# Performance work log

Measured on AMD Instinct MI355X. Metric: run time of the kernel, lower is better.

Reference implementation:

```python
import jax, jax.numpy as jnp
import numpy as np

N_ROLES = 6
EPS = 1e-5

def _ln(x, scale, bias):
    m = jnp.mean(x, axis=-1, keepdims=True)
    v = jnp.var(x, axis=-1, keepdims=True)
    return (x - m) * jax.lax.rsqrt(v + EPS) * scale + bias

def setup_inputs() -> dict:
    key = jax.random.key(0)
    ks = jax.random.split(key, 20)
    T, B, D_OBS, H, A = 32, 1024, 256, 512, 32
    inp = {
        'rnn_states': jax.random.normal(ks[0], (B, H), jnp.float32),
        'obs': jax.random.normal(ks[1], (T, B, D_OBS), jnp.float32),
        'resets': jnp.zeros((T, B), jnp.float32),
        'available_actions': jnp.ones((T, B, A), jnp.float32),
        'role_ids': jax.random.randint(ks[2], (T, B), 0, N_ROLES, jnp.int32),
        # feature norm over obs_dim
        'fn_scale': jnp.ones((D_OBS,), jnp.float32),
        'fn_bias': jnp.zeros((D_OBS,), jnp.float32),
        # base MLP: obs_dim->512->512, each followed by LayerNorm
        'W0': jax.random.normal(ks[3], (D_OBS, H), jnp.float32) * 0.02,
        'b0': jnp.zeros((H,), jnp.float32),
        'ln0_scale': jnp.ones((H,), jnp.float32),
        'ln0_bias': jnp.zeros((H,), jnp.float32),
        'W1': jax.random.normal(ks[4], (H, H), jnp.float32) * 0.02,
        'b1': jnp.zeros((H,), jnp.float32),
        'ln1_scale': jnp.ones((H,), jnp.float32),
        'ln1_bias': jnp.zeros((H,), jnp.float32),
        # per-role routes: obs_dim->128->H (stacked over roles)
        'Wr0': jax.random.normal(ks[5], (N_ROLES, D_OBS, 128), jnp.float32) * 0.02,
        'br0': jnp.zeros((N_ROLES, 128), jnp.float32),
        'Wr1': jax.random.normal(ks[6], (N_ROLES, 128, H), jnp.float32) * 0.02,
        'br1': jnp.zeros((N_ROLES, H), jnp.float32),
        # per-role heads: H->64->32->action_dim (stacked over roles)
        'Wh0': jax.random.normal(ks[7], (N_ROLES, H, 64), jnp.float32) * 0.02,
        'bh0': jnp.zeros((N_ROLES, 64), jnp.float32),
        'Wh1': jax.random.normal(ks[8], (N_ROLES, 64, 32), jnp.float32) * 0.02,
        'bh1': jnp.zeros((N_ROLES, 32), jnp.float32),
        'Wh2': jax.random.normal(ks[9], (N_ROLES, 32, A), jnp.float32) * 0.02,
        'bh2': jnp.zeros((N_ROLES, A), jnp.float32),
    }
    return inp

def _gather_by_role(all_values, role_ids):
    # all_values: (K, T, B, F); role_ids: (T, B) -> (T, B, F)
    idx = role_ids[None, :, :, None].astype(jnp.int32)
    return jnp.take_along_axis(all_values, idx, axis=0)[0]

def reference(rnn_states, obs, resets, available_actions, role_ids,
              fn_scale, fn_bias, W0, b0, ln0_scale, ln0_bias,
              W1, b1, ln1_scale, ln1_bias,
              Wr0, br0, Wr1, br1,
              Wh0, bh0, Wh1, bh1, Wh2, bh2):
    # feature normalization on raw obs
    obs_n = _ln(obs, fn_scale, fn_bias)
    # shared base MLP (relu + LayerNorm after each Dense)
    e = _ln(jax.nn.relu(obs_n @ W0 + b0), ln0_scale, ln0_bias)
    e = _ln(jax.nn.relu(e @ W1 + b1), ln1_scale, ln1_bias)
    # per-role pre-GRU residual routes on (normalized) obs
    r = jax.nn.relu(jnp.einsum('tbi,kih->ktbh', obs_n, Wr0) + br0[:, None, None, :])
    r = jax.nn.relu(jnp.einsum('ktbh,kho->ktbo', r, Wr1) + br1[:, None, None, :])
    e = e + _gather_by_role(r, role_ids)
    # no recurrent policy configured: rnn_states pass through
    # per-role heads -> all logits (K, T, B, A)
    h = jax.nn.relu(jnp.einsum('tbh,khf->ktbf', e, Wh0) + bh0[:, None, None, :])
    h = jax.nn.relu(jnp.einsum('ktbf,kfg->ktbg', h, Wh1) + bh1[:, None, None, :])
    all_logits = jnp.einsum('ktbg,kga->ktba', h, Wh2) + bh2[:, None, None, :]
    logits = _gather_by_role(all_logits, role_ids)
    logits = jnp.where(available_actions > 0.5, logits, jnp.full_like(logits, -1e10))
    return rnn_states, logits
```

## Files before the change

kernel.cpp:

```cpp
#include <hip/hip_runtime.h>
#include <stdint.h>

typedef unsigned short u16;
typedef unsigned int u32;

using bf16x8 = __attribute__((ext_vector_type(8))) short;
using f32x4  = __attribute__((ext_vector_type(4))) float;

#define DEVINL __device__ __forceinline__

DEVINL float b2f(u16 u) { return __builtin_bit_cast(float, (u32)u << 16); }
DEVINL u16 f2b(float f) {
  u32 u = __builtin_bit_cast(u32, f);
  u += 0x7FFFu + ((u >> 16) & 1u);
  return (u16)(u >> 16);
}

DEVINL void gll16(const u16* src, u16* dst) {
  __builtin_amdgcn_global_load_lds(
      (const __attribute__((address_space(1))) void*)(uintptr_t)src,
      (__attribute__((address_space(3))) void*)(uintptr_t)dst, 16, 0, 0);
}

DEVINL void tp_tile(const float* __restrict__ s, u16* __restrict__ d,
                    int R, int C, int bx, int by, int z)
{
  __shared__ u16 tile[32][33];
  const size_t mstride = (size_t)R * C;
  s += (size_t)z * mstride;
  d += (size_t)z * mstride;
  int r0 = bx * 32, c0 = by * 32;
  int tx = threadIdx.x & 31, ty = threadIdx.x >> 5;
#pragma unroll
  for (int i = 0; i < 32; i += 8)
    tile[ty + i][tx] = f2b(s[(size_t)(r0 + ty + i) * C + (c0 + tx)]);
  __syncthreads();
#pragma unroll
  for (int i = 0; i < 32; i += 8)
    d[(size_t)(c0 + ty + i) * R + (r0 + tx)] = tile[tx][ty + i];
}

__global__ __launch_bounds__(256) void transpose_all(
    const float* W0, const float* W1, const float* Wr0, const float* Wr1, const float* Wh0,
    u16* W0t, u16* W1t, u16* Wr0t, u16* Wr1t, u16* Wh0t)
{
  int b = blockIdx.x;
  if (b < 128)      {            tp_tile(W0, W0t, 256, 512, b % 8,  b / 8, 0); }
  else if (b < 384) { b -= 128;  tp_tile(W1, W1t, 512, 512, b % 16, b / 16, 0); }
  else if (b < 576) { b -= 384;  int t = b / 8;  tp_tile(Wr0, Wr0t, 256, 128, b % 8,  t % 4,  t / 4); }
  else if (b < 960) { b -= 576;  int t = b / 4;  tp_tile(Wr1, Wr1t, 128, 512, b % 4,  t % 16, t / 16); }
  else              { b -= 960;  int t = b / 16; tp_tile(Wh0, Wh0t, 512, 64,  b % 16, t % 2,  t / 2); }
}

__global__ __launch_bounds__(256) void ln_f32_256(
    const float* __restrict__ X, const float* __restrict__ sc,
    const float* __restrict__ bi, u16* __restrict__ Y, int nrows)
{
  constexpr int D = 256, PER = 4;
  int lane = threadIdx.x & 63;
  int row = blockIdx.x * 4 + (threadIdx.x >> 6);
  if (row >= nrows) return;
  const float* xr = X + (size_t)row * D + lane * PER;
  float x[PER] __attribute__((aligned(16)));
  *(float4*)x = *(const float4*)xr;
  float s = 0.f, s2 = 0.f;
#pragma unroll
  for (int p = 0; p < PER; ++p) { s += x[p]; s2 += x[p] * x[p]; }
#pragma unroll
  for (int o = 32; o > 0; o >>= 1) { s += __shfl_xor(s, o, 64); s2 += __shfl_xor(s2, o, 64); }
  float m = s * (1.f / D);
  float v = s2 * (1.f / D) - m * m;
  float inv = rsqrtf(v + 1e-5f);
  u16 yu[PER] __attribute__((aligned(8)));
#pragma unroll
  for (int p = 0; p < PER; ++p)
    yu[p] = f2b((x[p] - m) * inv * sc[lane * PER + p] + bi[lane * PER + p]);
  *(uint2*)(Y + (size_t)row * D + lane * PER) = *(uint2*)yu;
}

#define NROLE 6
__global__ __launch_bounds__(256) void role_count(
    const int* __restrict__ rid, int* __restrict__ blkCnt)
{
  __shared__ int h[NROLE];
  if (threadIdx.x < NROLE) h[threadIdx.x] = 0;
  __syncthreads();
  int i = blockIdx.x * 256 + threadIdx.x;
  atomicAdd(&h[rid[i]], 1);
  __syncthreads();
  if (threadIdx.x < NROLE) blkCnt[blockIdx.x * NROLE + threadIdx.x] = h[threadIdx.x];
}

__global__ __launch_bounds__(256) void role_scan(
    const int* __restrict__ blkCnt, int* __restrict__ blkBase,
    int* __restrict__ baseArr, int* __restrict__ cntArr)
{
  __shared__ int c[128 * NROLE];
  __shared__ int bb[128 * NROLE];
  __shared__ int sbase[NROLE], scnt[NROLE];
  for (int i = threadIdx.x; i < 128 * NROLE; i += 256) c[i] = blkCnt[i];
  __syncthreads();
  if (threadIdx.x < NROLE) {
    int k = threadIdx.x, run = 0;
    for (int b = 0; b < 128; ++b) { bb[b * NROLE + k] = run; run += c[b * NROLE + k]; }
    scnt[k] = run;
  }
  __syncthreads();
  if (threadIdx.x == 0) {
    int r = 0;
    for (int k = 0; k < NROLE; ++k) { sbase[k] = r; r += scnt[k]; }
  }
  __syncthreads();
  if (threadIdx.x < NROLE) { baseArr[threadIdx.x] = sbase[threadIdx.x]; cntArr[threadIdx.x] = scnt[threadIdx.x]; }
  for (int i = threadIdx.x; i < 128 * NROLE; i += 256)
    blkBase[i] = bb[i] + sbase[i % NROLE];
}

__global__ __launch_bounds__(256) void role_fill(
    const int* __restrict__ rid, const int* __restrict__ blkBase, int* __restrict__ bucket)
{
  __shared__ int h[NROLE];
  if (threadIdx.x < NROLE) h[threadIdx.x] = 0;
  __syncthreads();
  int i = blockIdx.x * 256 + threadIdx.x;
  int k = rid[i];
  int pos = atomicAdd(&h[k], 1);
  bucket[blkBase[blockIdx.x * NROLE + k] + pos] = i;
}

template <int K>
__global__ __launch_bounds__(256, 4) void gemm_ln(
    const u16* __restrict__ A, const u16* __restrict__ Bt,
    const float* __restrict__ bias, const float* __restrict__ lnsc,
    const float* __restrict__ lnbi, u16* __restrict__ C)
{
  constexpr int BK = 64;
  __shared__ __align__(16) u16 As[32 * BK];
  __shared__ float redS[32][4];
  __shared__ float redSS[32][4];
  __shared__ float prm[1536];
  const int tid = threadIdx.x;
  const int rowBase = blockIdx.x * 32;
  const int lane = tid & 63, wave = tid >> 6;
#pragma unroll
  for (int i = tid; i < 512; i += 256) {
    prm[i] = bias[i]; prm[512 + i] = lnsc[i]; prm[1024 + i] = lnbi[i];
  }
  const int srow = tid >> 3;
  const u32 aOff = (u32)(rowBase + srow) * (u32)K + (u32)(((tid & 7) ^ (srow & 7)) * 8);
  const int quad = lane >> 4, lm = lane & 15, l7 = lm & 7;
  const int wn = wave * 128;
  u32 bOff[8];
#pragma unroll
  for (int j = 0; j < 8; ++j)
    bOff[j] = (u32)(wn + j * 16 + lm) * (u32)K + (u32)(quad * 8);

  f32x4 acc[2][8] = {};

  for (int k0 = 0; k0 < K; k0 += BK) {
    gll16(A + aOff + k0, &As[wave * 512]);
    __syncthreads();
#pragma unroll
    for (int kk = 0; kk < BK; kk += 32) {
      const int kc = kk >> 3;
      bf16x8 af[2], bfr[8];
#pragma unroll
      for (int i2 = 0; i2 < 2; ++i2)
        af[i2] = *(const bf16x8*)&As[(i2 * 16 + lm) * 64 + (((quad + kc) ^ l7) * 8)];
#pragma unroll
      for (int j = 0; j < 8; ++j)
        bfr[j] = *(const bf16x8*)(Bt + bOff[j] + k0 + kk);
#pragma unroll
      for (int i2 = 0; i2 < 2; ++i2)
#pragma unroll
        for (int j = 0; j < 8; ++j)
          acc[i2][j] = __builtin_amdgcn_mfma_f32_16x16x32_bf16(af[i2], bfr[j], acc[i2][j], 0, 0, 0);
    }
    __syncthreads();
  }

#pragma unroll
  for (int i2 = 0; i2 < 2; ++i2) {
#pragma unroll
    for (int r2 = 0; r2 < 4; ++r2) {
      float s = 0.f, ss = 0.f;
#pragma unroll
      for (int j = 0; j < 8; ++j) {
        float v = fmaxf(acc[i2][j][r2] + prm[wn + j * 16 + lm], 0.f);
        acc[i2][j][r2] = v;
        s += v; ss += v * v;
      }
#pragma unroll
      for (int o = 1; o < 16; o <<= 1) { s += __shfl_xor(s, o, 64); ss += __shfl_xor(ss, o, 64); }
      if (lm == 0) {
        int rowL = i2 * 16 + quad * 4 + r2;
        redS[rowL][wave] = s;
        redSS[rowL][wave] = ss;
      }
    }
  }
  __syncthreads();
#pragma unroll
  for (int i2 = 0; i2 < 2; ++i2) {
#pragma unroll
    for (int r2 = 0; r2 < 4; ++r2) {
      int rowL = i2 * 16 + quad * 4 + r2;
      float ts  = redS[rowL][0] + redS[rowL][1] + redS[rowL][2] + redS[rowL][3];
      float tss = redSS[rowL][0] + redSS[rowL][1] + redSS[rowL][2] + redSS[rowL][3];
      float m = ts * (1.f / 512.f);
      float var = tss * (1.f / 512.f) - m * m;
      float inv = rsqrtf(var + 1e-5f);
      size_t base = (size_t)(rowBase + rowL) * 512;
#pragma unroll
      for (int j = 0; j < 8; ++j) {
        int col = wn + j * 16 + lm;
        float y = (acc[i2][j][r2] - m) * inv * prm[512 + col] + prm[1024 + col];
        C[base + col] = f2b(y);
      }
    }
  }
}

__global__ __launch_bounds__(256, 3) void route_head(
    const u16* __restrict__ obs_n, const u16* __restrict__ e,
    const u16* __restrict__ Wr0t, const float* __restrict__ br0,
    const u16* __restrict__ Wr1t, const float* __restrict__ br1,
    const u16* __restrict__ Wh0t, const float* __restrict__ bh0,
    const int* __restrict__ bucket, const int* __restrict__ baseArr,
    const int* __restrict__ cntArr, u16* __restrict__ h0buf)
{
  __shared__ __align__(16) u16 sm[20480];
  __shared__ float prm[704];
  const int tid = threadIdx.x;

  int role = 0, rem = blockIdx.x, cnt;
  for (;;) {
    cnt = cntArr[role];
    int tiles = (cnt + 31) >> 5;
    if (rem < tiles) break;
    rem -= tiles;
    if (++role >= NROLE) return;
  }
  const int limit = cnt;
  const int rowBase = rem * 32;
  const int roleBase = baseArr[role];

  {
    const float* s0 = br0 + role * 128;
    const float* s1 = br1 + role * 512;
    const float* s2 = bh0 + role * 64;
    if (tid < 128) prm[tid] = s0[tid];
    for (int i = tid; i < 512; i += 256) prm[128 + i] = s1[i];
    if (tid < 64) prm[640 + tid] = s2[tid];
  }

  const int lane = tid & 63, wave = tid >> 6;
  const int quad = lane >> 4, lm = lane & 15, l7 = lm & 7;

#pragma unroll
  for (int r = 0; r < 4; ++r) {
    int lrow = r * 8 + (tid >> 5);
    int i = rowBase + lrow;
    if (i >= limit) i = rowBase;
    int grow = bucket[roleBase + i];
    gll16(obs_n + (u32)grow * 256u + (u32)((((tid & 31) ^ (lrow & 7)) * 8)),
          &sm[r * 2048 + wave * 512]);
  }
  __syncthreads();

  const int wn0 = wave * 32;
  const u16* B0 = Wr0t + (size_t)role * 128 * 256;
  f32x4 acc0[2][2] = {};
#pragma unroll
  for (int kk = 0; kk < 256; kk += 32) {
    const int kc = kk >> 3;
    bf16x8 af[2], bf0[2];
#pragma unroll
    for (int i2 = 0; i2 < 2; ++i2)
      af[i2] = *(const bf16x8*)&sm[(i2 * 16 + lm) * 256 + (((quad + kc) ^ l7) * 8)];
#pragma unroll
    for (int j = 0; j < 2; ++j)
      bf0[j] = *(const bf16x8*)(B0 + (u32)(wn0 + j * 16 + lm) * 256u + (u32)(quad * 8 + kk));
#pragma unroll
    for (int i2 = 0; i2 < 2; ++i2)
#pragma unroll
      for (int j = 0; j < 2; ++j)
        acc0[i2][j] = __builtin_amdgcn_mfma_f32_16x16x32_bf16(af[i2], bf0[j], acc0[i2][j], 0, 0, 0);
  }
  u16* r1 = sm + 16384;
#pragma unroll
  for (int i2 = 0; i2 < 2; ++i2) {
#pragma unroll
    for (int r2 = 0; r2 < 4; ++r2) {
      int row = i2 * 16 + quad * 4 + r2;
#pragma unroll
      for (int j = 0; j < 2; ++j) {
        int col = wn0 + j * 16 + lm;
        float v = fmaxf(acc0[i2][j][r2] + prm[col], 0.f);
        r1[row * 128 + (((col >> 3) ^ (row & 7)) * 8) + (col & 7)] = f2b(v);
      }
    }
  }
  __syncthreads();

  const int wn1 = wave * 128;
  const u16* B1 = Wr1t + (size_t)role * 512 * 128;
  f32x4 acc1[2][8] = {};
#pragma unroll
  for (int kk = 0; kk < 128; kk += 32) {
    const int kc = kk >> 3;
    bf16x8 af[2], bf1[8];
#pragma unroll
    for (int i2 = 0; i2 < 2; ++i2)
      af[i2] = *(const bf16x8*)&r1[(i2 * 16 + lm) * 128 + (((quad + kc) ^ l7) * 8)];
#pragma unroll
    for (int j = 0; j < 8; ++j)
      bf1[j] = *(const bf16x8*)(B1 + (u32)(wn1 + j * 16 + lm) * 128u + (u32)(quad * 8 + kk));
#pragma unroll
    for (int i2 = 0; i2 < 2; ++i2)
#pragma unroll
      for (int j = 0; j < 8; ++j)
        acc1[i2][j] = __builtin_amdgcn_mfma_f32_16x16x32_bf16(af[i2], bf1[j], acc1[i2][j], 0, 0, 0);
  }
#pragma unroll
  for (int i2 = 0; i2 < 2; ++i2) {
#pragma unroll
    for (int r2 = 0; r2 < 4; ++r2) {
      int row = i2 * 16 + quad * 4 + r2;
      int i = rowBase + row;
      int ic = (i < limit) ? i : (limit - 1);
      u32 grow = (u32)bucket[roleBase + ic];
#pragma unroll
      for (int j = 0; j < 8; ++j) {
        int col = wn1 + j * 16 + lm;
        float v = fmaxf(acc1[i2][j][r2] + prm[128 + col], 0.f) + b2f(e[(size_t)grow * 512 + col]);
        sm[row * 512 + (((col >> 3) ^ (row & 7)) * 8) + (col & 7)] = f2b(v);
      }
    }
  }
  __syncthreads();

  const int wn2 = wave * 16;
  const u16* B2 = Wh0t + (size_t)role * 64 * 512;
  f32x4 acc2[2] = {};
#pragma unroll
  for (int kk = 0; kk < 512; kk += 32) {
    const int kc = kk >> 3;
    bf16x8 af[2], bf2;
#pragma unroll
    for (int i2 = 0; i2 < 2; ++i2)
      af[i2] = *(const bf16x8*)&sm[(i2 * 16 + lm) * 512 + (((quad + kc) ^ l7) * 8)];
    bf2 = *(const bf16x8*)(B2 + (u32)(wn2 + lm) * 512u + (u32)(quad * 8 + kk));
#pragma unroll
    for (int i2 = 0; i2 < 2; ++i2)
      acc2[i2] = __builtin_amdgcn_mfma_f32_16x16x32_bf16(af[i2], bf2, acc2[i2], 0, 0, 0);
  }
#pragma unroll
  for (int i2 = 0; i2 < 2; ++i2) {
#pragma unroll
    for (int r2 = 0; r2 < 4; ++r2) {
      int row = i2 * 16 + quad * 4 + r2;
      int i = rowBase + row;
      if (i >= limit) continue;
      int col = wn2 + lm;
      float v = fmaxf(acc2[i2][r2] + prm[640 + col], 0.f);
      h0buf[(size_t)(roleBase + i) * 64 + col] = f2b(v);
    }
  }
}

__global__ __launch_bounds__(256) void head_tail(
    const u16* __restrict__ h0buf, const int* __restrict__ bucket,
    const int* __restrict__ baseArr,
    const float* __restrict__ Wh1, const float* __restrict__ bh1,
    const float* __restrict__ Wh2, const float* __restrict__ bh2,
    const float* __restrict__ avail, float* __restrict__ outLogits)
{
  int lane = threadIdx.x & 63;
  int p = blockIdx.x * 4 + (threadIdx.x >> 6);
  int row = bucket[p];
  int k = 0;
#pragma unroll
  for (int j = 1; j < NROLE; ++j) k += (p >= baseArr[j]);
  float h0 = b2f(h0buf[(size_t)p * 64 + lane]);
  int n = lane & 31, half = lane >> 5;
  const float* W1k = Wh1 + k * 64 * 32;
  float a1 = 0.f;
#pragma unroll
  for (int jj = 0; jj < 32; ++jj) {
    int j = half * 32 + jj;
    float hj = __shfl(h0, j, 64);
    a1 += hj * W1k[j * 32 + n];
  }
  a1 += __shfl_xor(a1, 32, 64);
  float h1 = fmaxf(a1 + bh1[k * 32 + n], 0.f);
  const float* W2k = Wh2 + k * 32 * 32;
  float a2 = 0.f;
#pragma unroll
  for (int nn = 0; nn < 32; ++nn) {
    float hn = __shfl(h1, nn, 64);
    a2 += hn * W2k[nn * 32 + n];
  }
  float logit = a2 + bh2[k * 32 + n];
  float av = avail[(size_t)row * 32 + n];
  if (av <= 0.5f) logit = -1e10f;
  if (half == 0) outLogits[(size_t)row * 32 + n] = logit;
}

extern "C" void kernel_launch(void* const* d_in, const int* in_sizes, int n_in,
                              void* d_out, int out_size, void* d_ws, size_t ws_size,
                              hipStream_t stream)
{
  const float* rnn  = (const float*)d_in[0];
  const float* obs  = (const float*)d_in[1];
  const float* avail= (const float*)d_in[3];
  const int*   rid  = (const int*)d_in[4];
  const float* fn_s = (const float*)d_in[5];
  const float* fn_b = (const float*)d_in[6];
  const float* W0   = (const float*)d_in[7];
  const float* b0   = (const float*)d_in[8];
  const float* ln0s = (const float*)d_in[9];
  const float* ln0b = (const float*)d_in[10];
  const float* W1   = (const float*)d_in[11];
  const float* b1   = (const float*)d_in[12];
  const float* ln1s = (const float*)d_in[13];
  const float* ln1b = (const float*)d_in[14];
  const float* Wr0  = (const float*)d_in[15];
  const float* br0  = (const float*)d_in[16];
  const float* Wr1  = (const float*)d_in[17];
  const float* br1  = (const float*)d_in[18];
  const float* Wh0  = (const float*)d_in[19];
  const float* bh0  = (const float*)d_in[20];
  const float* Wh1  = (const float*)d_in[21];
  const float* bh1  = (const float*)d_in[22];
  const float* Wh2  = (const float*)d_in[23];
  const float* bh2  = (const float*)d_in[24];

  const int ROWS = 32768;

  char* w = (char*)d_ws;
  auto carve = [&](size_t bytes) { char* p = w; w += (bytes + 255) & ~(size_t)255; return p; };
  u16* obs_n  = (u16*)carve((size_t)ROWS * 256 * 2);
  u16* bufA   = (u16*)carve((size_t)ROWS * 512 * 2);
  u16* bufB   = (u16*)carve((size_t)ROWS * 512 * 2);
  u16* h0buf  = (u16*)carve((size_t)ROWS * 64 * 2);
  u16* W0t    = (u16*)carve((size_t)512 * 256 * 2);
  u16* W1t    = (u16*)carve((size_t)512 * 512 * 2);
  u16* Wr0t   = (u16*)carve((size_t)6 * 128 * 256 * 2);
  u16* Wr1t   = (u16*)carve((size_t)6 * 512 * 128 * 2);
  u16* Wh0t   = (u16*)carve((size_t)6 * 64 * 512 * 2);
  int* bucket = (int*)carve((size_t)ROWS * 4);
  int* blkCnt = (int*)carve((size_t)128 * NROLE * 4);
  int* blkBase= (int*)carve((size_t)128 * NROLE * 4);
  int* baseArr= (int*)carve(256);
  int* cntArr = (int*)carve(256);

  float* outLogits = (float*)d_out + (size_t)1024 * 512;

  hipMemcpyAsync(d_out, rnn, (size_t)1024 * 512 * 4, hipMemcpyDeviceToDevice, stream);

  transpose_all<<<1152, 256, 0, stream>>>(W0, W1, Wr0, Wr1, Wh0, W0t, W1t, Wr0t, Wr1t, Wh0t);

  ln_f32_256<<<8192, 256, 0, stream>>>(obs, fn_s, fn_b, obs_n, ROWS);

  role_count<<<128, 256, 0, stream>>>(rid, blkCnt);
  role_scan<<<1, 256, 0, stream>>>(blkCnt, blkBase, baseArr, cntArr);
  role_fill<<<128, 256, 0, stream>>>(rid, blkBase, bucket);

  gemm_ln<256><<<1024, 256, 0, stream>>>(obs_n, W0t, b0, ln0s, ln0b, bufA);
  gemm_ln<512><<<1024, 256, 0, stream>>>(bufA, W1t, b1, ln1s, ln1b, bufB);

  route_head<<<1029, 256, 0, stream>>>(obs_n, bufB, Wr0t, br0, Wr1t, br1, Wh0t, bh0,
                                       bucket, baseArr, cntArr, h0buf);

  head_tail<<<8192, 256, 0, stream>>>(h0buf, bucket, baseArr, Wh1, bh1, Wh2, bh2, avail, outLogits);
}
```

Baseline: 317.6 us.

## Double-buffer gemm_ln with 64-row tiles and fuse head tail into route_head

gemm_ln now handles 64 rows per block and double-buffers its LDS A tile. B fragments are prefetched one half-step ahead, so global loads overlap the MFMA work and the weight traffic per row is halved. The small head MLP (64->32->32), the availability masking and the scatter are folded into the end of route_head, working out of shared memory. This removes the h0buf round trip and the separate head_tail launch. In exchange, gemm_ln uses more registers and occupancy drops to 2 blocks per SIMD target, and the fused tail adds shared memory and a scalar FMA phase to route_head.

New measurement: 274.6 us. 1.16x faster.

```diff
diff --git a/kernel.cpp b/kernel.cpp
--- a/kernel.cpp
+++ b/kernel.cpp
@@ -129,25 +129,29 @@
 }
 
 template <int K>
-__global__ __launch_bounds__(256, 4) void gemm_ln(
+__global__ __launch_bounds__(256, 2) void gemm_ln(
     const u16* __restrict__ A, const u16* __restrict__ Bt,
     const float* __restrict__ bias, const float* __restrict__ lnsc,
     const float* __restrict__ lnbi, u16* __restrict__ C)
 {
-  constexpr int BK = 64;
-  __shared__ __align__(16) u16 As[32 * BK];
-  __shared__ float redS[32][4];
-  __shared__ float redSS[32][4];
+  constexpr int BK = 64, NI = K / BK;
+  __shared__ __align__(16) u16 As[2][64 * BK];
+  __shared__ float redS[64][4];
+  __shared__ float redSS[64][4];
   __shared__ float prm[1536];
   const int tid = threadIdx.x;
-  const int rowBase = blockIdx.x * 32;
+  const int rowBase = blockIdx.x * 64;
   const int lane = tid & 63, wave = tid >> 6;
 #pragma unroll
   for (int i = tid; i < 512; i += 256) {
     prm[i] = bias[i]; prm[512 + i] = lnsc[i]; prm[1024 + i] = lnbi[i];
   }
-  const int srow = tid >> 3;
-  const u32 aOff = (u32)(rowBase + srow) * (u32)K + (u32)(((tid & 7) ^ (srow & 7)) * 8);
+  u32 aOff[2];
+#pragma unroll
+  for (int r = 0; r < 2; ++r) {
+    int row = r * 32 + (tid >> 3);
+    aOff[r] = (u32)(rowBase + row) * (u32)K + (u32)(((tid & 7) ^ (row & 7)) * 8);
+  }
   const int quad = lane >> 4, lm = lane & 15, l7 = lm & 7;
   const int wn = wave * 128;
   u32 bOff[8];
@@ -155,32 +159,55 @@
   for (int j = 0; j < 8; ++j)
     bOff[j] = (u32)(wn + j * 16 + lm) * (u32)K + (u32)(quad * 8);
 
-  f32x4 acc[2][8] = {};
-
-  for (int k0 = 0; k0 < K; k0 += BK) {
-    gll16(A + aOff + k0, &As[wave * 512]);
+  f32x4 acc[4][8] = {};
+
+#pragma unroll
+  for (int r = 0; r < 2; ++r)
+    gll16(A + aOff[r], &As[0][r * 2048 + wave * 512]);
+  bf16x8 bP[8];
+#pragma unroll
+  for (int j = 0; j < 8; ++j)
+    bP[j] = *(const bf16x8*)(Bt + bOff[j]);
+  __syncthreads();
+
+  for (int i = 0; i < NI; ++i) {
+    const u16* Ab = As[i & 1];
+    if (i + 1 < NI) {
+#pragma unroll
+      for (int r = 0; r < 2; ++r)
+        gll16(A + aOff[r] + (i + 1) * BK, &As[(i + 1) & 1][r * 2048 + wave * 512]);
+    }
+    bf16x8 bN[8];
+#pragma unroll
+    for (int j = 0; j < 8; ++j)
+      bN[j] = *(const bf16x8*)(Bt + bOff[j] + i * BK + 32);
+    bf16x8 af[4];
+#pragma unroll
+    for (int i2 = 0; i2 < 4; ++i2)
+      af[i2] = *(const bf16x8*)&Ab[(i2 * 16 + lm) * 64 + ((quad ^ l7) * 8)];
+#pragma unroll
+    for (int i2 = 0; i2 < 4; ++i2)
+#pragma unroll
+      for (int j = 0; j < 8; ++j)
+        acc[i2][j] = __builtin_amdgcn_mfma_f32_16x16x32_bf16(af[i2], bP[j], acc[i2][j], 0, 0, 0);
+    if (i + 1 < NI) {
+#pragma unroll
+      for (int j = 0; j < 8; ++j)
+        bP[j] = *(const bf16x8*)(Bt + bOff[j] + (i + 1) * BK);
+    }
+#pragma unroll
+    for (int i2 = 0; i2 < 4; ++i2)
+      af[i2] = *(const bf16x8*)&Ab[(i2 * 16 + lm) * 64 + (((quad + 4) ^ l7) * 8)];
+#pragma unroll
+    for (int i2 = 0; i2 < 4; ++i2)
+#pragma unroll
+      for (int j = 0; j < 8; ++j)
+        acc[i2][j] = __builtin_amdgcn_mfma_f32_16x16x32_bf16(af[i2], bN[j], acc[i2][j], 0, 0, 0);
     __syncthreads();
-#pragma unroll
-    for (int kk = 0; kk < BK; kk += 32) {
-      const int kc = kk >> 3;
-      bf16x8 af[2], bfr[8];
-#pragma unroll
-      for (int i2 = 0; i2 < 2; ++i2)
-        af[i2] = *(const bf16x8*)&As[(i2 * 16 + lm) * 64 + (((quad + kc) ^ l7) * 8)];
-#pragma unroll
-      for (int j = 0; j < 8; ++j)
-        bfr[j] = *(const bf16x8*)(Bt + bOff[j] + k0 + kk);
-#pragma unroll
-      for (int i2 = 0; i2 < 2; ++i2)
-#pragma unroll
-        for (int j = 0; j < 8; ++j)
-          acc[i2][j] = __builtin_amdgcn_mfma_f32_16x16x32_bf16(af[i2], bfr[j], acc[i2][j], 0, 0, 0);
-    }
-    __syncthreads();
-  }
-
-#pragma unroll
-  for (int i2 = 0; i2 < 2; ++i2) {
+  }
+
+#pragma unroll
+  for (int i2 = 0; i2 < 4; ++i2) {
 #pragma unroll
     for (int r2 = 0; r2 < 4; ++r2) {
       float s = 0.f, ss = 0.f;
@@ -201,7 +228,7 @@
   }
   __syncthreads();
 #pragma unroll
-  for (int i2 = 0; i2 < 2; ++i2) {
+  for (int i2 = 0; i2 < 4; ++i2) {
 #pragma unroll
     for (int r2 = 0; r2 < 4; ++r2) {
       int rowL = i2 * 16 + quad * 4 + r2;
@@ -226,11 +253,15 @@
     const u16* __restrict__ Wr0t, const float* __restrict__ br0,
     const u16* __restrict__ Wr1t, const float* __restrict__ br1,
     const u16* __restrict__ Wh0t, const float* __restrict__ bh0,
+    const float* __restrict__ Wh1, const float* __restrict__ bh1,
+    const float* __restrict__ Wh2, const float* __restrict__ bh2,
+    const float* __restrict__ avail,
     const int* __restrict__ bucket, const int* __restrict__ baseArr,
-    const int* __restrict__ cntArr, u16* __restrict__ h0buf)
+    const int* __restrict__ cntArr, float* __restrict__ outLogits)
 {
   __shared__ __align__(16) u16 sm[20480];
   __shared__ float prm[704];
+  __shared__ float h1s[32 * 36];
   const int tid = threadIdx.x;
 
   int role = 0, rem = blockIdx.x, cnt;
@@ -355,56 +386,54 @@
     for (int i2 = 0; i2 < 2; ++i2)
       acc2[i2] = __builtin_amdgcn_mfma_f32_16x16x32_bf16(af[i2], bf2, acc2[i2], 0, 0, 0);
   }
+  u16* h0s = sm + 16384;
 #pragma unroll
   for (int i2 = 0; i2 < 2; ++i2) {
 #pragma unroll
     for (int r2 = 0; r2 < 4; ++r2) {
       int row = i2 * 16 + quad * 4 + r2;
-      int i = rowBase + row;
-      if (i >= limit) continue;
       int col = wn2 + lm;
-      float v = fmaxf(acc2[i2][r2] + prm[640 + col], 0.f);
-      h0buf[(size_t)(roleBase + i) * 64 + col] = f2b(v);
-    }
-  }
-}
-
-__global__ __launch_bounds__(256) void head_tail(
-    const u16* __restrict__ h0buf, const int* __restrict__ bucket,
-    const int* __restrict__ baseArr,
-    const float* __restrict__ Wh1, const float* __restrict__ bh1,
-    const float* __restrict__ Wh2, const float* __restrict__ bh2,
-    const float* __restrict__ avail, float* __restrict__ outLogits)
-{
-  int lane = threadIdx.x & 63;
-  int p = blockIdx.x * 4 + (threadIdx.x >> 6);
-  int row = bucket[p];
-  int k = 0;
-#pragma unroll
-  for (int j = 1; j < NROLE; ++j) k += (p >= baseArr[j]);
-  float h0 = b2f(h0buf[(size_t)p * 64 + lane]);
-  int n = lane & 31, half = lane >> 5;
-  const float* W1k = Wh1 + k * 64 * 32;
-  float a1 = 0.f;
-#pragma unroll
-  for (int jj = 0; jj < 32; ++jj) {
-    int j = half * 32 + jj;
-    float hj = __shfl(h0, j, 64);
-    a1 += hj * W1k[j * 32 + n];
-  }
-  a1 += __shfl_xor(a1, 32, 64);
-  float h1 = fmaxf(a1 + bh1[k * 32 + n], 0.f);
-  const float* W2k = Wh2 + k * 32 * 32;
-  float a2 = 0.f;
-#pragma unroll
-  for (int nn = 0; nn < 32; ++nn) {
-    float hn = __shfl(h1, nn, 64);
-    a2 += hn * W2k[nn * 32 + n];
-  }
-  float logit = a2 + bh2[k * 32 + n];
-  float av = avail[(size_t)row * 32 + n];
-  if (av <= 0.5f) logit = -1e10f;
-  if (half == 0) outLogits[(size_t)row * 32 + n] = logit;
+      h0s[row * 68 + col] = f2b(fmaxf(acc2[i2][r2] + prm[640 + col], 0.f));
+    }
+  }
+  __syncthreads();
+
+  {
+    const int r = tid >> 3;
+    const int n0 = (tid & 7) * 4;
+    const bool valid = (rowBase + r) < limit;
+    const float* W1k = Wh1 + (size_t)role * 64 * 32;
+    const float* W2k = Wh2 + (size_t)role * 32 * 32;
+    float4 a1 = *(const float4*)(bh1 + role * 32 + n0);
+#pragma unroll 8
+    for (int j = 0; j < 64; ++j) {
+      float hj = b2f(h0s[r * 68 + j]);
+      float4 wv = *(const float4*)(W1k + j * 32 + n0);
+      a1.x += hj * wv.x; a1.y += hj * wv.y; a1.z += hj * wv.z; a1.w += hj * wv.w;
+    }
+    h1s[r * 36 + n0 + 0] = fmaxf(a1.x, 0.f);
+    h1s[r * 36 + n0 + 1] = fmaxf(a1.y, 0.f);
+    h1s[r * 36 + n0 + 2] = fmaxf(a1.z, 0.f);
+    h1s[r * 36 + n0 + 3] = fmaxf(a1.w, 0.f);
+    __syncthreads();
+    float4 a2 = *(const float4*)(bh2 + role * 32 + n0);
+#pragma unroll 8
+    for (int n = 0; n < 32; ++n) {
+      float hn = h1s[r * 36 + n];
+      float4 wv = *(const float4*)(W2k + n * 32 + n0);
+      a2.x += hn * wv.x; a2.y += hn * wv.y; a2.z += hn * wv.z; a2.w += hn * wv.w;
+    }
+    if (valid) {
+      int g = bucket[roleBase + rowBase + r];
+      float4 av = *(const float4*)(avail + (size_t)g * 32 + n0);
+      float4 o;
+      o.x = (av.x > 0.5f) ? a2.x : -1e10f;
+      o.y = (av.y > 0.5f) ? a2.y : -1e10f;
+      o.z = (av.z > 0.5f) ? a2.z : -1e10f;
+      o.w = (av.w > 0.5f) ? a2.w : -1e10f;
+      *(float4*)(outLogits + (size_t)g * 32 + n0) = o;
+    }
+  }
 }
 
 extern "C" void kernel_launch(void* const* d_in, const int* in_sizes, int n_in,
@@ -443,7 +472,6 @@
   u16* obs_n  = (u16*)carve((size_t)ROWS * 256 * 2);
   u16* bufA   = (u16*)carve((size_t)ROWS * 512 * 2);
   u16* bufB   = (u16*)carve((size_t)ROWS * 512 * 2);
-  u16* h0buf  = (u16*)carve((size_t)ROWS * 64 * 2);
   u16* W0t    = (u16*)carve((size_t)512 * 256 * 2);
   u16* W1t    = (u16*)carve((size_t)512 * 512 * 2);
   u16* Wr0t   = (u16*)carve((size_t)6 * 128 * 256 * 2);
@@ -467,11 +495,10 @@
   role_scan<<<1, 256, 0, stream>>>(blkCnt, blkBase, baseArr, cntArr);
   role_fill<<<128, 256, 0, stream>>>(rid, blkBase, bucket);
 
-  gemm_ln<256><<<1024, 256, 0, stream>>>(obs_n, W0t, b0, ln0s, ln0b, bufA);
-  gemm_ln<512><<<1024, 256, 0, stream>>>(bufA, W1t, b1, ln1s, ln1b, bufB);
+  gemm_ln<256><<<512, 256, 0, stream>>>(obs_n, W0t, b0, ln0s, ln0b, bufA);
+  gemm_ln<512><<<512, 256, 0, stream>>>(bufA, W1t, b1, ln1s, ln1b, bufB);
 
   route_head<<<1029, 256, 0, stream>>>(obs_n, bufB, Wr0t, br0, Wr1t, br1, Wh0t, bh0,
-                                       bucket, baseArr, cntArr, h0buf);
-
-  head_tail<<<8192, 256, 0, stream>>>(h0buf, bucket, baseArr, Wh1, bh1, Wh2, bh2, avail, outLogits);
-}
+                                       Wh1, bh1, Wh2, bh2, avail,
+                                       bucket, baseArr, cntArr, outLogits);
+}
```
